# Kernel tuning notes

Measured on AMD Instinct MI355X. Metric: run time of the kernel, lower is better.

The kernel has to match this reference:

```python
import jax, jax.numpy as jnp
import numpy as np

N, K, H = 2048, 128, 512
TOPK = 8
EPS = 1e-12  # torch F.normalize eps


def _l2_normalize(x):
    # matches F.normalize(x, dim=-1): x / max(||x||_2, eps)
    n = jnp.sqrt(jnp.sum(x * x, axis=-1, keepdims=True))
    return x / jnp.maximum(n, EPS)


def setup_inputs() -> dict:
    key = jax.random.key(0)
    k1, k2, k3, k4 = jax.random.split(key, 4)
    q = jax.random.normal(k1, (N, H), dtype=jnp.float32)
    mem_k = jax.random.normal(k2, (N, K, H), dtype=jnp.float32)
    mem_v = jax.random.normal(k3, (N, K, H), dtype=jnp.float32)
    mem_m = (jax.random.uniform(k4, (N, K)) > 0.3).astype(jnp.float32)
    return {"q": q, "mem_k": mem_k, "mem_v": mem_v, "mem_m": mem_m}


def reference(q, mem_k, mem_v, mem_m):
    qn = _l2_normalize(q)                      # [N, H]
    kn = _l2_normalize(mem_k)                  # [N, K, H]
    sim = jnp.einsum('nh,nkh->nk', qn, kn)     # [N, K] cosine sims
    sim = jnp.where(mem_m <= 0.0, jnp.float32(-1e9), sim)
    k = min(TOPK, K)
    vals, idx = jax.lax.top_k(sim, k)          # [N, k]
    attn = jax.nn.softmax(vals, axis=1)        # [N, k]
    v_sel = jnp.take_along_axis(mem_v, idx[:, :, None], axis=1)  # [N, k, H]
    out = jnp.einsum('nk,nkh->nh', attn, v_sel)                  # [N, H]
    return out
```

## Files before the change

kernel.cpp:

```cpp
#include <hip/hip_runtime.h>
#include <math.h>

#define KK   128
#define HH   512
#define TOPK 8

__global__ __launch_bounds__(256) void lm_kernel(
    const float* __restrict__ q,
    const float* __restrict__ mem_k,
    const float* __restrict__ mem_v,
    const float* __restrict__ mem_m,
    float* __restrict__ out)
{
    const int n    = blockIdx.x;
    const int tid  = threadIdx.x;
    const int wave = tid >> 6;
    const int lane = tid & 63;

    __shared__ float s_sim[KK];
    __shared__ float s_attn[TOPK];
    __shared__ int   s_idx[TOPK];

    const float4* qv = (const float4*)(q + (size_t)n * HH) + lane * 2;
    const float4 qa = qv[0];
    const float4 qb = qv[1];

    float qss = qa.x*qa.x + qa.y*qa.y + qa.z*qa.z + qa.w*qa.w
              + qb.x*qb.x + qb.y*qb.y + qb.z*qb.z + qb.w*qb.w;
    #pragma unroll
    for (int m = 1; m < 64; m <<= 1) qss += __shfl_xor(qss, m, 64);
    const float qn = fmaxf(sqrtf(qss), 1e-12f);

    const float* kbase = mem_k + (size_t)n * KK * HH;
    const float* mrow  = mem_m + (size_t)n * KK;
    const int k0 = wave * 32;
    for (int k = k0; k < k0 + 32; ++k) {
        const float4* kv = (const float4*)(kbase + (size_t)k * HH) + lane * 2;
        const float4 ka = kv[0];
        const float4 kb = kv[1];
        float dot = qa.x*ka.x + qa.y*ka.y + qa.z*ka.z + qa.w*ka.w
                  + qb.x*kb.x + qb.y*kb.y + qb.z*kb.z + qb.w*kb.w;
        float kss = ka.x*ka.x + ka.y*ka.y + ka.z*ka.z + ka.w*ka.w
                  + kb.x*kb.x + kb.y*kb.y + kb.z*kb.z + kb.w*kb.w;
        #pragma unroll
        for (int m = 1; m < 64; m <<= 1) {
            dot += __shfl_xor(dot, m, 64);
            kss += __shfl_xor(kss, m, 64);
        }
        if (lane == 0) {
            const float kn  = fmaxf(sqrtf(kss), 1e-12f);
            float sim = dot / (qn * kn);
            if (mrow[k] <= 0.0f) sim = -1e9f;
            s_sim[k] = sim;
        }
    }
    __syncthreads();

    if (wave == 0) {
        float va = s_sim[lane];
        float vb = s_sim[lane + 64];
        float topv[TOPK];
        int   topi[TOPK];
        #pragma unroll
        for (int j = 0; j < TOPK; ++j) {
            float bv; int bi;
            if (vb > va) { bv = vb; bi = lane + 64; }
            else         { bv = va; bi = lane; }
            #pragma unroll
            for (int m = 1; m < 64; m <<= 1) {
                const float ov = __shfl_xor(bv, m, 64);
                const int   oi = __shfl_xor(bi, m, 64);
                if (ov > bv || (ov == bv && oi < bi)) { bv = ov; bi = oi; }
            }
            topv[j] = bv; topi[j] = bi;
            if (bi == lane)      va = -INFINITY;
            if (bi == lane + 64) vb = -INFINITY;
        }
        float e[TOPK];
        float ssum = 0.0f;
        #pragma unroll
        for (int j = 0; j < TOPK; ++j) { e[j] = expf(topv[j] - topv[0]); ssum += e[j]; }
        if (lane == 0) {
            const float inv = 1.0f / ssum;
            #pragma unroll
            for (int j = 0; j < TOPK; ++j) { s_attn[j] = e[j] * inv; s_idx[j] = topi[j]; }
        }
    }
    __syncthreads();

    const float* vbase = mem_v + (size_t)n * KK * HH;
    const int h = tid * 2;
    float acc0 = 0.0f, acc1 = 0.0f;
    #pragma unroll
    for (int j = 0; j < TOPK; ++j) {
        const float  a  = s_attn[j];
        const float2 vv = *(const float2*)(vbase + (size_t)s_idx[j] * HH + h);
        acc0 += a * vv.x;
        acc1 += a * vv.y;
    }
    float2 o; o.x = acc0; o.y = acc1;
    *(float2*)(out + (size_t)n * HH + h) = o;
}

extern "C" void kernel_launch(void* const* d_in, const int* in_sizes, int n_in,
                              void* d_out, int out_size, void* d_ws, size_t ws_size,
                              hipStream_t stream) {
    const float* q     = (const float*)d_in[0];
    const float* mem_k = (const float*)d_in[1];
    const float* mem_v = (const float*)d_in[2];
    const float* mem_m = (const float*)d_in[3];
    float* out = (float*)d_out;
    const int n_rows = in_sizes[0] / HH;
    lm_kernel<<<n_rows, 256, 0, stream>>>(q, mem_k, mem_v, mem_m, out);
}
```

Before: 894.1 us.

## Split waves into 16-lane groups and double-buffer key row loads

```diff
diff --git a/kernel.cpp b/kernel.cpp
--- a/kernel.cpp
+++ b/kernel.cpp
@@ -16,40 +16,65 @@
     const int tid  = threadIdx.x;
     const int wave = tid >> 6;
     const int lane = tid & 63;
+    const int g    = lane >> 4;
+    const int s    = lane & 15;
 
     __shared__ float s_sim[KK];
     __shared__ float s_attn[TOPK];
     __shared__ int   s_idx[TOPK];
 
-    const float4* qv = (const float4*)(q + (size_t)n * HH) + lane * 2;
-    const float4 qa = qv[0];
-    const float4 qb = qv[1];
+    const float* qrow = q + (size_t)n * HH;
+    float4 qv[8];
+    #pragma unroll
+    for (int j = 0; j < 8; ++j)
+        qv[j] = *(const float4*)(qrow + j * 64 + s * 4);
 
-    float qss = qa.x*qa.x + qa.y*qa.y + qa.z*qa.z + qa.w*qa.w
-              + qb.x*qb.x + qb.y*qb.y + qb.z*qb.z + qb.w*qb.w;
+    float qss = 0.0f;
     #pragma unroll
-    for (int m = 1; m < 64; m <<= 1) qss += __shfl_xor(qss, m, 64);
+    for (int j = 0; j < 8; ++j)
+        qss += qv[j].x*qv[j].x + qv[j].y*qv[j].y + qv[j].z*qv[j].z + qv[j].w*qv[j].w;
+    #pragma unroll
+    for (int m = 1; m < 16; m <<= 1) qss += __shfl_xor(qss, m, 16);
     const float qn = fmaxf(sqrtf(qss), 1e-12f);
 
     const float* kbase = mem_k + (size_t)n * KK * HH;
     const float* mrow  = mem_m + (size_t)n * KK;
     const int k0 = wave * 32;
-    for (int k = k0; k < k0 + 32; ++k) {
-        const float4* kv = (const float4*)(kbase + (size_t)k * HH) + lane * 2;
-        const float4 ka = kv[0];
-        const float4 kb = kv[1];
-        float dot = qa.x*ka.x + qa.y*ka.y + qa.z*ka.z + qa.w*ka.w
-                  + qb.x*kb.x + qb.y*kb.y + qb.z*kb.z + qb.w*kb.w;
-        float kss = ka.x*ka.x + ka.y*ka.y + ka.z*ka.z + ka.w*ka.w
-                  + kb.x*kb.x + kb.y*kb.y + kb.z*kb.z + kb.w*kb.w;
+
+    float4 bufA[8], bufB[8];
+    {
+        const float* p = kbase + (size_t)(k0 + g) * HH + s * 4;
         #pragma unroll
-        for (int m = 1; m < 64; m <<= 1) {
-            dot += __shfl_xor(dot, m, 64);
-            kss += __shfl_xor(kss, m, 64);
+        for (int j = 0; j < 8; ++j) bufA[j] = *(const float4*)(p + j * 64);
+    }
+
+    #pragma unroll
+    for (int i = 0; i < 8; ++i) {
+        const float4* cur = (i & 1) ? bufB : bufA;
+        float4*       nxt = (i & 1) ? bufA : bufB;
+        if (i < 7) {
+            const float* p = kbase + (size_t)(k0 + (i + 1) * 4 + g) * HH + s * 4;
+            #pragma unroll
+            for (int j = 0; j < 8; ++j) nxt[j] = *(const float4*)(p + j * 64);
         }
-        if (lane == 0) {
-            const float kn  = fmaxf(sqrtf(kss), 1e-12f);
-            float sim = dot / (qn * kn);
+        float d0 = 0.0f, d1 = 0.0f, ks0 = 0.0f, ks1 = 0.0f;
+        #pragma unroll
+        for (int j = 0; j < 8; j += 2) {
+            d0  += qv[j].x*cur[j].x + qv[j].y*cur[j].y + qv[j].z*cur[j].z + qv[j].w*cur[j].w;
+            ks0 += cur[j].x*cur[j].x + cur[j].y*cur[j].y + cur[j].z*cur[j].z + cur[j].w*cur[j].w;
+            d1  += qv[j+1].x*cur[j+1].x + qv[j+1].y*cur[j+1].y + qv[j+1].z*cur[j+1].z + qv[j+1].w*cur[j+1].w;
+            ks1 += cur[j+1].x*cur[j+1].x + cur[j+1].y*cur[j+1].y + cur[j+1].z*cur[j+1].z + cur[j+1].w*cur[j+1].w;
+        }
+        float dot = d0 + d1;
+        float kss = ks0 + ks1;
+        #pragma unroll
+        for (int m = 1; m < 16; m <<= 1) {
+            dot += __shfl_xor(dot, m, 16);
+            kss += __shfl_xor(kss, m, 16);
+        }
+        if (s == 0) {
+            const int k = k0 + i * 4 + g;
+            float sim = dot / (qn * fmaxf(sqrtf(kss), 1e-12f));
             if (mrow[k] <= 0.0f) sim = -1e9f;
             s_sim[k] = sim;
         }
```

Result: no change. 891.0 us (-0.4%).
